# Kernel optimization log

Measured on AMD Instinct MI355X. Metric: run time of the kernel, lower is better.

The kernel has to match this reference:

```python
import jax, jax.numpy as jnp
import numpy as np

N = 30000      # nodes
E = 480000     # edges
G = 256        # g_dim
H = 8          # heads
D = G // H     # head dim
SCALE = G ** (-0.5)
LN_EPS = 1e-5


def setup_inputs() -> dict:
    key = jax.random.key(0)
    k0, k1, k2, k3 = jax.random.split(key, 4)
    s = jax.random.normal(k0, (N, G), dtype=jnp.float32)
    src = jax.random.randint(k1, (E,), 0, N, dtype=jnp.int32)
    dst = jax.random.randint(k2, (E,), 0, N, dtype=jnp.int32)
    # learned params: fused qkv projection (no bias) + LayerNorm affine
    Wqkv = jax.random.normal(k3, (G, 3 * G), dtype=jnp.float32) * (G ** -0.5)
    gamma = jnp.ones((G,), dtype=jnp.float32)
    beta = jnp.zeros((G,), dtype=jnp.float32)
    return {"s": s, "Wqkv": Wqkv, "gamma": gamma, "beta": beta, "src": src, "dst": dst}


def _segment_softmax(logits, seg, num_segments):
    # numerically stable softmax over edges grouped by destination node,
    # elementwise over trailing (h, d) dims — matches dgl.edge_softmax
    m = jax.ops.segment_max(logits, seg, num_segments=num_segments)
    e = jnp.exp(logits - m[seg])
    z = jax.ops.segment_sum(e, seg, num_segments=num_segments)
    return e / z[seg]


def reference(s, Wqkv, gamma, beta, src, dst):
    # LayerNorm over feature dim
    mu = jnp.mean(s, axis=-1, keepdims=True)
    var = jnp.mean((s - mu) ** 2, axis=-1, keepdims=True)
    x = (s - mu) * jax.lax.rsqrt(var + LN_EPS) * gamma + beta
    # fused qkv projection, split into heads
    qkv = x @ Wqkv                                  # [N, 3G]
    q, k, v = jnp.split(qkv, 3, axis=-1)
    q = q.reshape(N, H, D)
    k = k.reshape(N, H, D)
    v = v.reshape(N, H, D)
    # per-edge elementwise attention: u_mul_v('q','k') * scale -> [E, H, D]
    att = q[src] * k[dst] * SCALE
    att = _segment_softmax(att, dst, N)
    # weighted scatter-sum aggregation: sum_e v[src_e] * att_e into dst_e
    msg = v[src] * att                              # [E, H, D]
    rst = jax.ops.segment_sum(msg, dst, num_segments=N)  # [N, H, D]
    return rst.reshape(N, G)
```

## Files before the change

### kernel.cpp

```cpp
#include <hip/hip_runtime.h>
#include <hip/hip_fp16.h>
#include <string.h>

#define NN 30000
#define NE 480000
#define CAP 96
#define KSC (0.0625f * 1.44269504f)

typedef __attribute__((ext_vector_type(8))) _Float16 f16x8;
typedef __attribute__((ext_vector_type(4))) float f32x4;
typedef __attribute__((ext_vector_type(4))) int i32x4;
typedef __attribute__((ext_vector_type(2))) unsigned int u32x2;

__device__ __forceinline__ unsigned short f2h(float f) {
    _Float16 h = (_Float16)f;
    unsigned short u;
    memcpy(&u, &h, 2);
    return u;
}

__device__ __forceinline__ void gload16(const void* g, void* l) {
    __builtin_amdgcn_global_load_lds(
        (const __attribute__((address_space(1))) unsigned int*)g,
        (__attribute__((address_space(3))) unsigned int*)l, 16, 0, 0);
}

__global__ __launch_bounds__(256) void prologue_kernel(const float* __restrict__ s,
                                                       const float* __restrict__ gamma,
                                                       const float* __restrict__ beta,
                                                       unsigned short* __restrict__ xh,
                                                       const float* __restrict__ W,
                                                       unsigned short* __restrict__ WT,
                                                       int* __restrict__ cur,
                                                       unsigned int* __restrict__ colu,
                                                       unsigned int* __restrict__ qvu) {
    const int bid = blockIdx.x;
    if (bid < NN) {
        const int n = bid;
        const int c = threadIdx.x;
        float v = s[n * 256 + c];
        float sum = v, sq = v * v;
        for (int o = 32; o; o >>= 1) {
            sum += __shfl_down(sum, o, 64);
            sq  += __shfl_down(sq,  o, 64);
        }
        __shared__ float ssum[4], ssq[4];
        const int wave = c >> 6, lane = c & 63;
        if (lane == 0) { ssum[wave] = sum; ssq[wave] = sq; }
        __syncthreads();
        float ts = ssum[0] + ssum[1] + ssum[2] + ssum[3];
        float tq = ssq[0]  + ssq[1]  + ssq[2]  + ssq[3];
        float mu  = ts * (1.0f / 256.0f);
        float var = tq * (1.0f / 256.0f) - mu * mu;
        float x = (v - mu) * rsqrtf(var + 1e-5f) * gamma[c] + beta[c];
        xh[n * 256 + c] = f2h(x);
    } else if (bid < NN + 768) {
        const int idx = (bid - NN) * 256 + threadIdx.x;
        const int n = idx >> 8;
        const int k = idx & 255;
        WT[idx] = f2h(W[k * 768 + n]);
    } else {
        const int i = (bid - NN - 768) * 256 + threadIdx.x;
        const unsigned int sent2 = (unsigned int)NN | ((unsigned int)NN << 16);
        if (i < NN * CAP / 2) colu[i] = sent2;
        if (i < NN) cur[i] = 0;
        if (i < 8 * 32) {
            const int x = i >> 5, j = i & 31;
            qvu[((size_t)x * (NN + 1) + NN) * 32 + j] = 0u;
        }
    }
}

__global__ __launch_bounds__(256) void scatter_kernel(const int* __restrict__ src,
                                                      const int* __restrict__ dst,
                                                      int* __restrict__ cursor,
                                                      unsigned short* __restrict__ col) {
    const int e = blockIdx.x * 256 + threadIdx.x;
    if (e < NE) {
        const int d = dst[e];
        const int slot = atomicAdd(&cursor[d], 1);
        if (slot < CAP) col[d * CAP + slot] = (unsigned short)src[e];
    }
}

#define BM 128
#define BN 128
#define BK 64
#define CSTRIDE 136
#define MTILES 235

__global__ __launch_bounds__(256) void gemm_kernel(const unsigned short* __restrict__ A,
                                                   const unsigned short* __restrict__ B,
                                                   unsigned short* __restrict__ qv,
                                                   unsigned short* __restrict__ kb) {
    const int f   = blockIdx.x;
    const int xcd = f & 7;
    const int i   = f >> 3;
    const int bmi = xcd * 30 + i / 6;
    if (bmi >= MTILES) return;
    const int bm = bmi * BM;
    const int by = i % 6;
    const int bn = by * BN;

    __shared__ unsigned short smem[BM * CSTRIDE];
    unsigned short* As = smem;
    unsigned short* Bs = smem + 8192;

    const int tid  = threadIdx.x;
    const int lane = tid & 63;
    const int wave = tid >> 6;
    const int wm = (wave & 1) * 64;
    const int wn = (wave >> 1) * 64;
    const int l16  = lane & 15;
    const int quad = lane >> 4;

    const int srow0 = wave * 8 + (lane >> 3);
    const int ko    = (lane & 7) * 8;

    f32x4 acc[4][4] = {};

    for (int kt = 0; kt < 256; kt += BK) {
        #pragma unroll
        for (int j = 0; j < 4; j++) {
            const int r = srow0 + 32 * j;
            int gmA = bm + r; if (gmA >= NN) gmA = NN - 1;
            gload16(A + (size_t)gmA * 256 + kt + ko, &As[(wave * 8 + 32 * j) * 64]);
            gload16(B + (size_t)(bn + r) * 256 + kt + ko, &Bs[(wave * 8 + 32 * j) * 64]);
        }
        __syncthreads();

        #pragma unroll
        for (int ks = 0; ks < 2; ks++) {
            f16x8 af[4], bfr[4];
            #pragma unroll
            for (int ii = 0; ii < 4; ii++)
                af[ii]  = *(const f16x8*)(&As[(wm + ii * 16 + l16) * 64 + ks * 32 + quad * 8]);
            #pragma unroll
            for (int jj = 0; jj < 4; jj++)
                bfr[jj] = *(const f16x8*)(&Bs[(wn + jj * 16 + l16) * 64 + ks * 32 + quad * 8]);
            #pragma unroll
            for (int ii = 0; ii < 4; ii++)
                #pragma unroll
                for (int jj = 0; jj < 4; jj++)
                    acc[ii][jj] = __builtin_amdgcn_mfma_f32_16x16x32_f16(af[ii], bfr[jj], acc[ii][jj], 0, 0, 0);
        }
        __syncthreads();
    }

    #pragma unroll
    for (int ii = 0; ii < 4; ii++)
        #pragma unroll
        for (int jj = 0; jj < 4; jj++)
            #pragma unroll
            for (int r = 0; r < 4; r++)
                smem[(wm + ii * 16 + quad * 4 + r) * CSTRIDE + wn + jj * 16 + l16] =
                    f2h(acc[ii][jj][r]);
    __syncthreads();

    const int sector  = by >> 1;
    const int colhalf = (by & 1) * 128;
    const int row  = tid >> 1;
    const int cseg = (tid & 1) * 64;
    const int grow = bm + row;
    if (grow < NN) {
        #pragma unroll
        for (int k = 0; k < 8; k++) {
            i32x4 val = *(const i32x4*)(&smem[row * CSTRIDE + cseg + k * 8]);
            const int c = colhalf + cseg + k * 8;
            const int x = c >> 5;
            if (sector == 1) {
                *(i32x4*)(kb + ((size_t)x * NN + grow) * 32 + (c & 31)) = val;
            } else {
                unsigned short* base = qv + ((size_t)x * (NN + 1) + grow) * 64
                                       + ((c & 31) >> 2) * 8 + (sector == 2 ? 4 : 0);
                u32x2 lo, hi;
                lo.x = (unsigned int)val[0]; lo.y = (unsigned int)val[1];
                hi.x = (unsigned int)val[2]; hi.y = (unsigned int)val[3];
                *(u32x2*)(base)     = lo;
                *(u32x2*)(base + 8) = hi;
            }
        }
    }
}

#define SSTRIDE 100

__global__ __launch_bounds__(256) void edge_kernel(const unsigned short* __restrict__ qv,
                                                   const unsigned short* __restrict__ ks,
                                                   const int* __restrict__ cursor,
                                                   const unsigned short* __restrict__ col,
                                                   float* __restrict__ out) {
    const int x   = blockIdx.x;
    const int nb  = blockIdx.y * 32;
    const int tid = threadIdx.x;
    const int w   = tid >> 6;
    const int lane = tid & 63;

    __shared__ int scol[32 * SSTRIDE];
    __shared__ int sdegR[32], sdegS[32], snode[32];

    if (tid < 32) {
        const int n0 = nb + tid;
        int d = (n0 < NN) ? cursor[n0] : 0;
        sdegR[tid] = (d > CAP) ? CAP : d;
    }
    __syncthreads();
    if (tid < 32) {
        const int d = sdegR[tid];
        int r = 0;
        #pragma unroll
        for (int j = 0; j < 32; ++j) {
            const int dj = sdegR[j];
            r += (dj < d) || (dj == d && j < tid);
        }
        sdegS[r] = d;
        snode[r] = nb + tid;
    }
    __syncthreads();
    {
        const unsigned int* colu = (const unsigned int*)col;
        #pragma unroll
        for (int j = 0; j < 6; j++) {
            const int t2 = tid + j * 256;
            const int nd = t2 / 48;
            const int ps = t2 - nd * 48;
            const int sn = snode[nd];
            const int row = (sn < NN) ? sn : 0;
            const unsigned int u = colu[row * 48 + ps];
            scol[nd * SSTRIDE + 2 * ps]     = (int)(u & 0xffffu) << 7;
            scol[nd * SSTRIDE + 2 * ps + 1] = (int)(u >> 16) << 7;
        }
    }
    __syncthreads();

    const int g  = lane >> 3;
    const int cq = lane & 7;
    const int li = w * 8 + g;
    const int m  = snode[li];
    const int msafe = (m < NN) ? m : 0;

    const int mydeg = sdegS[li];
    const int dmax4 = (sdegS[w * 8 + 7] + 3) & ~3;

    union U { unsigned int u; __half2 h; };
    u32x2 kraw = *(const u32x2*)(ks + ((size_t)x * NN + msafe) * 32 + 4 * cq);
    U t0, t1; t0.u = kraw.x; t1.u = kraw.y;
    const __half2 ksc2 = __float2half2_rn(KSC);
    const __half2 kkA = __hmul2(t0.h, ksc2);
    const __half2 kkB = __hmul2(t1.h, ksc2);

    const char* qvp = (const char*)qv + (size_t)x * (NN + 1) * 128 + cq * 16;
    const int* myscol = &scol[li * SSTRIDE];

    __half2 zA = __float2half2_rn(0.0f), zB = __float2half2_rn(0.0f);
    __half2 aA = __float2half2_rn(0.0f), aB = __float2half2_rn(0.0f);

    for (int i = 0; i < dmax4; i += 4) {
        const i32x4 off4 = *(const i32x4*)(&myscol[i]);
        #pragma unroll
        for (int j = 0; j < 4; j++) {
            const i32x4 d4 = *(const i32x4*)(qvp + off4[j]);
            U q01, q23, v01, v23;
            q01.u = (unsigned int)d4[0];
            q23.u = (unsigned int)d4[1];
            v01.u = (unsigned int)d4[2];
            v23.u = (unsigned int)d4[3];
            const __half2 w0 = h2exp2(__hmul2(q01.h, kkA));
            const __half2 w1 = h2exp2(__hmul2(q23.h, kkB));
            zA = __hadd2(zA, w0);
            aA = __hfma2(w0, v01.h, aA);
            zB = __hadd2(zB, w1);
            aB = __hfma2(w1, v23.h, aB);
        }
    }

    const float npad = (float)(dmax4 - mydeg);
    f32x4 o;
    const float z0 = __low2float(zA)  - npad;
    const float z1 = __high2float(zA) - npad;
    const float z2 = __low2float(zB)  - npad;
    const float z3 = __high2float(zB) - npad;
    o[0] = (mydeg > 0) ? __low2float(aA)  / z0 : 0.0f;
    o[1] = (mydeg > 0) ? __high2float(aA) / z1 : 0.0f;
    o[2] = (mydeg > 0) ? __low2float(aB)  / z2 : 0.0f;
    o[3] = (mydeg > 0) ? __high2float(aB) / z3 : 0.0f;
    if (m < NN)
        *(f32x4*)(out + (size_t)m * 256 + x * 32 + 4 * cq) = o;
}

extern "C" void kernel_launch(void* const* d_in, const int* in_sizes, int n_in,
                              void* d_out, int out_size, void* d_ws, size_t ws_size,
                              hipStream_t stream) {
    const float* s     = (const float*)d_in[0];
    const float* Wqkv  = (const float*)d_in[1];
    const float* gamma = (const float*)d_in[2];
    const float* beta  = (const float*)d_in[3];
    const int*   src   = (const int*)d_in[4];
    const int*   dst   = (const int*)d_in[5];
    float* out = (float*)d_out;

    char* ws = (char*)d_ws;
    unsigned short* xh   = (unsigned short*)(ws);
    unsigned short* WT   = (unsigned short*)(ws + 15360000);
    unsigned short* qv   = (unsigned short*)(ws + 15753216);
    unsigned short* ks   = (unsigned short*)(ws + 46474240);
    int*            cur  = (int*)(ws + 61834240);
    unsigned short* col  = (unsigned short*)(ws + 61954240);

    const int init_blocks = (NN * CAP / 2 + 255) / 256;
    prologue_kernel<<<NN + 768 + init_blocks, 256, 0, stream>>>(
        s, gamma, beta, xh, Wqkv, WT, cur,
        (unsigned int*)col, (unsigned int*)qv);
    scatter_kernel<<<(NE + 255) / 256, 256, 0, stream>>>(src, dst, cur, col);
    gemm_kernel<<<1440, 256, 0, stream>>>(xh, WT, qv, ks);
    edge_kernel<<<dim3(8, (NN + 31) / 32), 256, 0, stream>>>(qv, ks, cur, col, out);
}
```

Measured before the change: 208.6 us.

## Fuse scatter into prologue, vectorize LayerNorm, tile W transpose, prefetch edge loads

Moves the edge scatter into the prologue launch and drops the full sentinel init of the column buffer. Padding entries are now masked to the zero sentinel row in the edge kernel based on degree. LayerNorm uses one wave per row with float4 loads and xor shuffles, and the weight transpose goes through a shared-memory tile. The edge loop is software-pipelined so the next four gathers are issued before computing the current ones. This removes a kernel launch and a large memset-like write, at the cost of a memset call, more registers in the edge loop, and reliance on degree masking for correctness.

```diff
diff --git a/kernel.cpp b/kernel.cpp
--- a/kernel.cpp
+++ b/kernel.cpp
@@ -25,61 +25,69 @@
         (__attribute__((address_space(3))) unsigned int*)l, 16, 0, 0);
 }
 
+#define LNB 7500
+#define WTB 48
 __global__ __launch_bounds__(256) void prologue_kernel(const float* __restrict__ s,
                                                        const float* __restrict__ gamma,
                                                        const float* __restrict__ beta,
                                                        unsigned short* __restrict__ xh,
                                                        const float* __restrict__ W,
                                                        unsigned short* __restrict__ WT,
-                                                       int* __restrict__ cur,
-                                                       unsigned int* __restrict__ colu,
+                                                       const int* __restrict__ src,
+                                                       const int* __restrict__ dst,
+                                                       int* __restrict__ cursor,
+                                                       unsigned short* __restrict__ col,
                                                        unsigned int* __restrict__ qvu) {
     const int bid = blockIdx.x;
-    if (bid < NN) {
-        const int n = bid;
-        const int c = threadIdx.x;
-        float v = s[n * 256 + c];
-        float sum = v, sq = v * v;
-        for (int o = 32; o; o >>= 1) {
-            sum += __shfl_down(sum, o, 64);
-            sq  += __shfl_down(sq,  o, 64);
-        }
-        __shared__ float ssum[4], ssq[4];
-        const int wave = c >> 6, lane = c & 63;
-        if (lane == 0) { ssum[wave] = sum; ssq[wave] = sq; }
+    const int tid = threadIdx.x;
+    if (bid < LNB) {
+        const int wave = tid >> 6, lane = tid & 63;
+        const int n = bid * 4 + wave;
+        const f32x4 v = *(const f32x4*)(s + (size_t)n * 256 + lane * 4);
+        float sum = v[0] + v[1] + v[2] + v[3];
+        float sq  = v[0]*v[0] + v[1]*v[1] + v[2]*v[2] + v[3]*v[3];
+        #pragma unroll
+        for (int o = 1; o < 64; o <<= 1) {
+            sum += __shfl_xor(sum, o, 64);
+            sq  += __shfl_xor(sq,  o, 64);
+        }
+        const float mu  = sum * (1.0f / 256.0f);
+        const float var = sq  * (1.0f / 256.0f) - mu * mu;
+        const float rs  = rsqrtf(var + 1e-5f);
+        const f32x4 g4 = *(const f32x4*)(gamma + lane * 4);
+        const f32x4 b4 = *(const f32x4*)(beta  + lane * 4);
+        union { unsigned short us[4]; u32x2 u; } o_;
+        #pragma unroll
+        for (int j = 0; j < 4; j++)
+            o_.us[j] = f2h((v[j] - mu) * rs * g4[j] + b4[j]);
+        *(u32x2*)(xh + (size_t)n * 256 + lane * 4) = o_.u;
+    } else if (bid < LNB + WTB) {
+        const int t  = bid - LNB;
+        const int k0 = (t & 3) * 64;
+        const int n0 = (t >> 2) * 64;
+        __shared__ float tsm[64][65];
+        const int tx = tid & 63, ty = tid >> 6;
+        #pragma unroll
+        for (int r = 0; r < 16; r++) {
+            const int kr = ty + r * 4;
+            tsm[kr][tx] = W[(size_t)(k0 + kr) * 768 + n0 + tx];
+        }
         __syncthreads();
-        float ts = ssum[0] + ssum[1] + ssum[2] + ssum[3];
-        float tq = ssq[0]  + ssq[1]  + ssq[2]  + ssq[3];
-        float mu  = ts * (1.0f / 256.0f);
-        float var = tq * (1.0f / 256.0f) - mu * mu;
-        float x = (v - mu) * rsqrtf(var + 1e-5f) * gamma[c] + beta[c];
-        xh[n * 256 + c] = f2h(x);
-    } else if (bid < NN + 768) {
-        const int idx = (bid - NN) * 256 + threadIdx.x;
-        const int n = idx >> 8;
-        const int k = idx & 255;
-        WT[idx] = f2h(W[k * 768 + n]);
+        #pragma unroll
+        for (int r = 0; r < 16; r++) {
+            const int nr = ty + r * 4;
+            WT[(size_t)(n0 + nr) * 256 + k0 + tx] = f2h(tsm[tx][nr]);
+        }
+    } else if (bid == LNB + WTB) {
+        const int x = tid >> 5, j = tid & 31;
+        qvu[((size_t)x * (NN + 1) + NN) * 32 + j] = 0u;
     } else {
-        const int i = (bid - NN - 768) * 256 + threadIdx.x;
-        const unsigned int sent2 = (unsigned int)NN | ((unsigned int)NN << 16);
-        if (i < NN * CAP / 2) colu[i] = sent2;
-        if (i < NN) cur[i] = 0;
-        if (i < 8 * 32) {
-            const int x = i >> 5, j = i & 31;
-            qvu[((size_t)x * (NN + 1) + NN) * 32 + j] = 0u;
-        }
-    }
-}
-
-__global__ __launch_bounds__(256) void scatter_kernel(const int* __restrict__ src,
-                                                      const int* __restrict__ dst,
-                                                      int* __restrict__ cursor,
-                                                      unsigned short* __restrict__ col) {
-    const int e = blockIdx.x * 256 + threadIdx.x;
-    if (e < NE) {
-        const int d = dst[e];
-        const int slot = atomicAdd(&cursor[d], 1);
-        if (slot < CAP) col[d * CAP + slot] = (unsigned short)src[e];
+        const int e = (bid - (LNB + WTB + 1)) * 256 + tid;
+        if (e < NE) {
+            const int d = dst[e];
+            const int slot = atomicAdd(&cursor[d], 1);
+            if (slot < CAP) col[d * CAP + slot] = (unsigned short)src[e];
+        }
     }
 }
 
@@ -185,6 +193,8 @@
 
 #define SSTRIDE 100
 
+union U { unsigned int u; __half2 h; };
+
 __global__ __launch_bounds__(256) void edge_kernel(const unsigned short* __restrict__ qv,
                                                    const unsigned short* __restrict__ ks,
                                                    const int* __restrict__ cursor,
@@ -225,10 +235,15 @@
             const int nd = t2 / 48;
             const int ps = t2 - nd * 48;
             const int sn = snode[nd];
+            const int deg = sdegS[nd];
             const int row = (sn < NN) ? sn : 0;
             const unsigned int u = colu[row * 48 + ps];
-            scol[nd * SSTRIDE + 2 * ps]     = (int)(u & 0xffffu) << 7;
-            scol[nd * SSTRIDE + 2 * ps + 1] = (int)(u >> 16) << 7;
+            int e0 = (int)(u & 0xffffu);
+            int e1 = (int)(u >> 16);
+            e0 = (2 * ps     < deg) ? e0 : NN;
+            e1 = (2 * ps + 1 < deg) ? e1 : NN;
+            scol[nd * SSTRIDE + 2 * ps]     = e0 << 7;
+            scol[nd * SSTRIDE + 2 * ps + 1] = e1 << 7;
         }
     }
     __syncthreads();
@@ -242,7 +257,6 @@
     const int mydeg = sdegS[li];
     const int dmax4 = (sdegS[w * 8 + 7] + 3) & ~3;
 
-    union U { unsigned int u; __half2 h; };
     u32x2 kraw = *(const u32x2*)(ks + ((size_t)x * NN + msafe) * 32 + 4 * cq);
     U t0, t1; t0.u = kraw.x; t1.u = kraw.y;
     const __half2 ksc2 = __float2half2_rn(KSC);
@@ -255,24 +269,40 @@
     __half2 zA = __float2half2_rn(0.0f), zB = __float2half2_rn(0.0f);
     __half2 aA = __float2half2_rn(0.0f), aB = __float2half2_rn(0.0f);
 
-    for (int i = 0; i < dmax4; i += 4) {
-        const i32x4 off4 = *(const i32x4*)(&myscol[i]);
-        #pragma unroll
-        for (int j = 0; j < 4; j++) {
-            const i32x4 d4 = *(const i32x4*)(qvp + off4[j]);
-            U q01, q23, v01, v23;
-            q01.u = (unsigned int)d4[0];
-            q23.u = (unsigned int)d4[1];
-            v01.u = (unsigned int)d4[2];
-            v23.u = (unsigned int)d4[3];
-            const __half2 w0 = h2exp2(__hmul2(q01.h, kkA));
-            const __half2 w1 = h2exp2(__hmul2(q23.h, kkB));
-            zA = __hadd2(zA, w0);
-            aA = __hfma2(w0, v01.h, aA);
-            zB = __hadd2(zB, w1);
-            aB = __hfma2(w1, v23.h, aB);
-        }
-    }
+#define EDGE_COMPUTE(d4) do {                                        \
+        U q01, q23, v01, v23;                                        \
+        q01.u = (unsigned int)(d4)[0];                               \
+        q23.u = (unsigned int)(d4)[1];                               \
+        v01.u = (unsigned int)(d4)[2];                               \
+        v23.u = (unsigned int)(d4)[3];                               \
+        const __half2 w0 = h2exp2(__hmul2(q01.h, kkA));              \
+        const __half2 w1 = h2exp2(__hmul2(q23.h, kkB));              \
+        zA = __hadd2(zA, w0);                                        \
+        aA = __hfma2(w0, v01.h, aA);                                 \
+        zB = __hadd2(zB, w1);                                        \
+        aB = __hfma2(w1, v23.h, aB);                                 \
+    } while (0)
+
+    if (dmax4 > 0) {
+        i32x4 off4 = *(const i32x4*)(&myscol[0]);
+        i32x4 dc0 = *(const i32x4*)(qvp + off4[0]);
+        i32x4 dc1 = *(const i32x4*)(qvp + off4[1]);
+        i32x4 dc2 = *(const i32x4*)(qvp + off4[2]);
+        i32x4 dc3 = *(const i32x4*)(qvp + off4[3]);
+        for (int i = 4; i < dmax4; i += 4) {
+            const i32x4 offn = *(const i32x4*)(&myscol[i]);
+            const i32x4 dn0 = *(const i32x4*)(qvp + offn[0]);
+            const i32x4 dn1 = *(const i32x4*)(qvp + offn[1]);
+            const i32x4 dn2 = *(const i32x4*)(qvp + offn[2]);
+            const i32x4 dn3 = *(const i32x4*)(qvp + offn[3]);
+            EDGE_COMPUTE(dc0); EDGE_COMPUTE(dc1);
+            EDGE_COMPUTE(dc2); EDGE_COMPUTE(dc3);
+            dc0 = dn0; dc1 = dn1; dc2 = dn2; dc3 = dn3;
+        }
+        EDGE_COMPUTE(dc0); EDGE_COMPUTE(dc1);
+        EDGE_COMPUTE(dc2); EDGE_COMPUTE(dc3);
+    }
+#undef EDGE_COMPUTE
 
     const float npad = (float)(dmax4 - mydeg);
     f32x4 o;
@@ -307,11 +337,11 @@
     int*            cur  = (int*)(ws + 61834240);
     unsigned short* col  = (unsigned short*)(ws + 61954240);
 
-    const int init_blocks = (NN * CAP / 2 + 255) / 256;
-    prologue_kernel<<<NN + 768 + init_blocks, 256, 0, stream>>>(
-        s, gamma, beta, xh, Wqkv, WT, cur,
-        (unsigned int*)col, (unsigned int*)qv);
-    scatter_kernel<<<(NE + 255) / 256, 256, 0, stream>>>(src, dst, cur, col);
+    hipMemsetAsync(cur, 0, NN * sizeof(int), stream);
+
+    const int scatter_blocks = (NE + 255) / 256;
+    prologue_kernel<<<LNB + WTB + 1 + scatter_blocks, 256, 0, stream>>>(
+        s, gamma, beta, xh, Wqkv, WT, src, dst, cur, col, (unsigned int*)qv);
     gemm_kernel<<<1440, 256, 0, stream>>>(xh, WT, qv, ks);
     edge_kernel<<<dim3(8, (NN + 31) / 32), 256, 0, stream>>>(qv, ks, cur, col, out);
 }
```

Measured after the change: 200.6 us. -3.8%, faster.
